# Kernel tuning notes

Hardware: AMD Instinct MI355X
Metric: run time of the kernel (lower is better)

## Reference

```python
import jax, jax.numpy as jnp
import numpy as np

BN_EPS = 1e-5


def _conv2d(x, w, b, pad):
    # x: [B,C,H,W], w: [O,I,kh,kw] (OIHW)
    y = jax.lax.conv_general_dilated(
        x, w, window_strides=(1, 1), padding=[(pad, pad), (pad, pad)],
        dimension_numbers=('NCHW', 'OIHW', 'NCHW'))
    return y + b[None, :, None, None]


def setup_inputs() -> dict:
    key = jax.random.key(0)
    ks = jax.random.split(key, 4)
    B, C, D, H, W = 8, 256, 1, 64, 64
    dm = 256
    x = jax.random.normal(ks[0], (B, C, D, H, W), dtype=jnp.float32)
    wq = jax.random.normal(ks[1], (dm, dm, 1, 1), dtype=jnp.float32) * 0.05
    bq = jnp.zeros((dm,), jnp.float32)
    wkv = jax.random.normal(ks[2], (2 * dm, dm, 3, 3), dtype=jnp.float32) * 0.05
    bkv = jnp.zeros((2 * dm,), jnp.float32)
    gamma = jnp.ones((dm,), jnp.float32)
    beta = jnp.zeros((dm,), jnp.float32)
    return {"x": x, "wq": wq, "bq": bq, "wkv": wkv, "bkv": bkv,
            "gamma": gamma, "beta": beta}


def reference(x, wq, bq, wkv, bkv, gamma, beta):
    B = x.shape[0]
    H, W = x.shape[-2], x.shape[-1]
    xc = x.reshape(B, -1, H, W)            # 'b c d h w -> b (c d) h w'
    dm = xc.shape[1]
    q = jax.nn.relu(_conv2d(xc, wq, bq, 0))       # [B,dm,H,W]
    kv = jax.nn.relu(_conv2d(xc, wkv, bkv, 1))    # [B,2dm,H,W]
    k, v = jnp.split(kv, 2, axis=1)

    def tok(t):  # 'b c x y -> b (x y) c'
        return t.transpose(0, 2, 3, 1).reshape(B, H * W, dm)

    qt, kt, vt = tok(q), tok(k), tok(v)
    sim = jnp.einsum('bid,bjd->bij', qt, kt)       # [B,N,N]
    A = jax.nn.softmax(sim / jnp.sqrt(jnp.float32(dm)), axis=-1)
    r = jnp.einsum('bij,bjd->bid', A, vt)          # [B,N,dm]
    r = r.reshape(B, H, W, dm).transpose(0, 3, 1, 2)  # 'b (x y) c -> b c x y'
    y = r + xc
    # BatchNorm2d, training mode: batch stats over (B,H,W), biased variance
    mean = jnp.mean(y, axis=(0, 2, 3), keepdims=True)
    var = jnp.var(y, axis=(0, 2, 3), keepdims=True)
    out = (y - mean) * jax.lax.rsqrt(var + BN_EPS)
    out = out * gamma[None, :, None, None] + beta[None, :, None, None]
    return out
```

## Files before the change

### kernel.cpp

```cpp
#include <hip/hip_runtime.h>


typedef __attribute__((ext_vector_type(8))) short bf16x8;
typedef __attribute__((ext_vector_type(4))) float f32x4;
typedef __attribute__((ext_vector_type(16))) float f32x16;
typedef __attribute__((ext_vector_type(8))) unsigned short u16x8;

__device__ inline unsigned short f2bf(float f) {
  union { float f; unsigned u; } c; c.f = f;
  unsigned u = c.u;
  return (unsigned short)((u + 0x7fffu + ((u >> 16) & 1u)) >> 16);
}

__device__ inline unsigned cvtpk(float lo, float hi) {
  unsigned r;
  asm("v_cvt_pk_bf16_f32 %0, %1, %2" : "=v"(r) : "v"(lo), "v"(hi));
  return r;
}

__device__ inline void dma16(const void* g, void* l) {
  __builtin_amdgcn_global_load_lds(
      (const __attribute__((address_space(1))) unsigned int*)g,
      (__attribute__((address_space(3))) unsigned int*)l, 16, 0, 0);
}

__global__ __launch_bounds__(256) void k_xt(
    const float* __restrict__ x, ushort* __restrict__ xt)
{
  const int b = blockIdx.z, ci0 = blockIdx.y * 64, gx = blockIdx.x;
  const int t = threadIdx.x;
  ushort* img = xt + (size_t)b * 4224 * 256;
  if (gx >= 64) {
    int r0 = (gx == 64) ? 0 : 4160;
#pragma unroll
    for (int k = 0; k < 2; ++k) {
      int idx = t + k * 256;
      int r = idx >> 3, u = idx & 7;
      u16x8 z = (u16x8)0;
      *(u16x8*)&img[(size_t)(r0 + r) * 256 + ci0 + u * 8] = z;
    }
    return;
  }
  const int n0 = gx * 64;
  __shared__ ushort tl[64][65];
  {
    const float* xb = x + ((size_t)b * 256 + ci0) * 4096 + n0;
    int i = t >> 2, j0 = (t & 3) * 16;
#pragma unroll
    for (int jj = 0; jj < 16; jj += 4) {
      float4 v = *(const float4*)&xb[(size_t)i * 4096 + j0 + jj];
      tl[j0 + jj + 0][i] = f2bf(v.x);
      tl[j0 + jj + 1][i] = f2bf(v.y);
      tl[j0 + jj + 2][i] = f2bf(v.z);
      tl[j0 + jj + 3][i] = f2bf(v.w);
    }
  }
  __syncthreads();
  {
    int j = t >> 3, u = t & 7;
#pragma unroll
    for (int k = 0; k < 2; ++k) {
      int jr = j + k * 32;
      ushort tmp[8];
#pragma unroll
      for (int e = 0; e < 8; ++e) tmp[e] = tl[jr][u * 8 + e];
      *(u16x8*)&img[(size_t)(64 + n0 + jr) * 256 + ci0 + u * 8] = *(u16x8*)tmp;
    }
  }
}

__global__ __launch_bounds__(256) void k_wprep(
    const float* __restrict__ w, ushort* __restrict__ wt, int ntaps, int nco)
{
  const int co = blockIdx.x;
  const int t = threadIdx.x;
  __shared__ float ws[2304];
  const int tot = 256 * ntaps;
  for (int i = t; i < tot; i += 256) ws[i] = w[(size_t)co * tot + i];
  __syncthreads();
  for (int tap = 0; tap < ntaps; ++tap)
    wt[((size_t)tap * nco + co) * 256 + t] = f2bf(ws[t * ntaps + tap]);
}

__global__ __launch_bounds__(256, 2) void k_conv(
    const ushort* __restrict__ xt, const ushort* __restrict__ wt,
    const float* __restrict__ bias, ushort* __restrict__ outT,
    ushort* __restrict__ outV, int ntaps, int nco, float oscale)
{
  extern __shared__ unsigned char smem[];
  ushort* As0 = (ushort*)smem;
  ushort* As1 = (ushort*)(smem + 16512);
  ushort* Bs0 = (ushort*)(smem + 33024);
  ushort* Bs1 = (ushort*)(smem + 33024 + 16384);
  __shared__ float bias_s[256];

  const int t = threadIdx.x, lane = t & 63;
  const int wv = t >> 6, wm = wv >> 1, wn = wv & 1;
  const int qc = lane & 15, grp = lane >> 4;
  const int b = blockIdx.z, n0 = blockIdx.x * 128, co0 = blockIdx.y * 256;
  const bool nchw = (outV != nullptr) && (blockIdx.y == 1);
  const ushort* img = xt + (size_t)b * 4224 * 256 + (size_t)64 * 256;
  const int wbase = t & ~63;

  bias_s[t] = bias[co0 + t];

  f32x4 acc[4][8];
#pragma unroll
  for (int mi = 0; mi < 4; ++mi)
#pragma unroll
    for (int ni = 0; ni < 8; ++ni) acc[mi][ni] = f32x4{0.f, 0.f, 0.f, 0.f};

  auto stageA = [&](int c8, ushort* dst) {
    const int ci0 = c8 * 32;
#pragma unroll
    for (int k = 0; k < 5; ++k) {
      int idx = k * 256 + t;
      if (idx < 1032) {
        int r = idx >> 2, u = idx & 3;
        int n = min(max(n0 + r - 65, -64), 4159);
        dma16(img + (size_t)n * 256 + ci0 + u * 8,
              dst + (size_t)(k * 256 + wbase) * 8);
      }
    }
  };
  auto stageB = [&](int tap, int c8, ushort* dst) {
    const ushort* wrow = wt + ((size_t)tap * nco + co0) * 256 + c8 * 32;
#pragma unroll
    for (int k = 0; k < 4; ++k) {
      int idx = k * 256 + t;
      int r = idx >> 2, u = idx & 3;
      dma16(wrow + (size_t)r * 256 + u * 8,
            dst + (size_t)(k * 256 + wbase) * 8);
    }
  };

  stageA(0, As0);
  stageB(0, 0, Bs0);
  asm volatile("s_waitcnt vmcnt(0)" ::: "memory");
  __syncthreads();

  const int niters = 8 * ntaps;
  int iter = 0;
  for (int c8 = 0; c8 < 8; ++c8) {
    const ushort* Asb = (c8 & 1) ? As1 : As0;
    for (int tap = 0; tap < ntaps; ++tap, ++iter) {
      const ushort* Bsb = (iter & 1) ? Bs1 : Bs0;
      if (iter + 1 < niters) {
        int ntap = (tap + 1 == ntaps) ? 0 : tap + 1;
        int nc8  = (tap + 1 == ntaps) ? c8 + 1 : c8;
        stageB(ntap, nc8, (iter & 1) ? Bs0 : Bs1);
        if (ntap == 0) stageA(nc8, (c8 & 1) ? As0 : As1);
      }
      const int dy = (ntaps == 9) ? (tap / 3 - 1) : 0;
      const int dx = (ntaps == 9) ? (tap % 3 - 1) : 0;
      const int off = dy * 64 + dx;
      bf16x8 bf[8];
#pragma unroll
      for (int ni = 0; ni < 8; ++ni)
        bf[ni] = *(const bf16x8*)&Bsb[(wn * 128 + ni * 16 + qc) * 32 + grp * 8];
#pragma unroll
      for (int mi = 0; mi < 4; ++mi) {
        int ar = wm * 64 + mi * 16 + qc + off + 65;
        bf16x8 af = *(const bf16x8*)&Asb[ar * 32 + grp * 8];
        if (dx < 0 && mi == 0 && qc == 0)  af = (bf16x8)0;
        if (dx > 0 && mi == 3 && qc == 15) af = (bf16x8)0;
#pragma unroll
        for (int ni = 0; ni < 8; ++ni)
          acc[mi][ni] = __builtin_amdgcn_mfma_f32_16x16x32_bf16(af, bf[ni], acc[mi][ni], 0, 0, 0);
      }
      asm volatile("s_waitcnt vmcnt(0)" ::: "memory");
      __syncthreads();
    }
  }

  if (!nchw) {
    ushort (*olds)[264] = (ushort(*)[264])smem;
#pragma unroll
    for (int mi = 0; mi < 4; ++mi) {
      int p = wm * 64 + mi * 16 + grp * 4;
#pragma unroll
      for (int ni = 0; ni < 8; ++ni) {
        int c = wn * 128 + ni * 16 + qc;
        float bv = bias_s[c];
#pragma unroll
        for (int r = 0; r < 4; ++r)
          olds[p + r][c] = f2bf(fmaxf(acc[mi][ni][r] + bv, 0.f) * oscale);
      }
    }
    __syncthreads();
    ushort* dst = outT + ((size_t)b * 4096 + n0) * 256;
#pragma unroll
    for (int k = 0; k < 16; ++k) {
      int idx = t + k * 256;
      int r = idx >> 5, u = idx & 31;
      *(u16x8*)&dst[(size_t)r * 256 + u * 8] = *(const u16x8*)&olds[r][u * 8];
    }
  } else {
    ushort (*oldsT)[136] = (ushort(*)[136])smem;
#pragma unroll
    for (int mi = 0; mi < 4; ++mi) {
      int p = wm * 64 + mi * 16 + grp * 4;
#pragma unroll
      for (int ni = 0; ni < 8; ++ni) {
        int c = wn * 128 + ni * 16 + qc;
        float bv = bias_s[c];
        ushort4 pk;
        pk.x = f2bf(fmaxf(acc[mi][ni][0] + bv, 0.f) * oscale);
        pk.y = f2bf(fmaxf(acc[mi][ni][1] + bv, 0.f) * oscale);
        pk.z = f2bf(fmaxf(acc[mi][ni][2] + bv, 0.f) * oscale);
        pk.w = f2bf(fmaxf(acc[mi][ni][3] + bv, 0.f) * oscale);
        *(ushort4*)&oldsT[c][p] = pk;
      }
    }
    __syncthreads();
    ushort* dst = outV + (size_t)b * 256 * 4096 + n0;
#pragma unroll
    for (int k = 0; k < 16; ++k) {
      int idx = t + k * 256;
      int c = idx >> 4, u = idx & 15;
      *(u16x8*)&dst[(size_t)c * 4096 + u * 8] = *(const u16x8*)&oldsT[c][u * 8];
    }
  }
}

__global__ __launch_bounds__(256, 1) void k_attn(
    const ushort* __restrict__ q_t, const ushort* __restrict__ k_t,
    const ushort* __restrict__ v_t, const float* __restrict__ x,
    float* __restrict__ y, float* __restrict__ gstat)
{
  extern __shared__ unsigned char smem[];
  ushort* kbf0 = (ushort*)smem;
  ushort* kbf1 = (ushort*)(smem + 32768);
  ushort* vbf0 = (ushort*)(smem + 65536);
  ushort* vbf1 = (ushort*)(smem + 98304);

  const int tid = threadIdx.x, lane = tid & 63, w = tid >> 6;
  const int q32 = lane & 31, gK = lane >> 5, swz = lane & 7;
  const int b = blockIdx.y, q0 = blockIdx.x * 128;
  const int wbase = tid & ~63;

  int offk[8], offv[8];
#pragma unroll
  for (int k = 0; k < 8; ++k) {
    int i = k * 256 + tid;
    int j = i >> 5, s = i & 31;
    offk[k] = j * 256 + ((s ^ (j & 7)) << 3);
    int d = i >> 3, s2 = i & 7;
    offv[k] = d * 4096 + ((s2 ^ (d & 7)) << 3);
  }
  const ushort* kT = k_t + (size_t)b * 4096 * 256;
  const ushort* vT = v_t + (size_t)b * 256 * 4096;

  bf16x8 qf[16];
  {
    const ushort* qrow =
        q_t + ((size_t)b * 4096 + q0 + w * 32 + q32) * 256 + gK * 8;
#pragma unroll
    for (int ds = 0; ds < 16; ++ds)
      qf[ds] = *(const bf16x8*)&qrow[ds * 16];
  }

  f32x16 o[8];
#pragma unroll
  for (int db = 0; db < 8; ++db) o[db] = (f32x16)0.f;
  float m_run = -1e30f, lp = 0.f;

  auto stage = [&](const ushort* kp, const ushort* vp, ushort* kb, ushort* vb) {
#pragma unroll
    for (int k = 0; k < 8; ++k)
      dma16(kp + offk[k], kb + (size_t)(k * 256 + wbase) * 8);
#pragma unroll
    for (int k = 0; k < 8; ++k)
      dma16(vp + offv[k], vb + (size_t)(k * 256 + wbase) * 8);
  };

  stage(kT, vT, kbf0, vbf0);
  kT += 16384; vT += 64;
  asm volatile("s_waitcnt vmcnt(0)" ::: "memory");
  __syncthreads();

  int kcol[16], vcol[4];
#pragma unroll
  for (int ds = 0; ds < 16; ++ds) kcol[ds] = ((2 * ds + gK) ^ swz) << 3;
#pragma unroll
  for (int ks = 0; ks < 4; ++ks) vcol[ks] = ((2 * ks + gK) ^ swz) << 3;
  const int krow0 = q32 * 256, krow1 = (q32 + 32) * 256;

  for (int t = 0; t < 64; ++t) {
    ushort* kb = (t & 1) ? kbf1 : kbf0;
    ushort* vb = (t & 1) ? vbf1 : vbf0;
    if (t < 63) {
      stage(kT, vT, (t & 1) ? kbf0 : kbf1, (t & 1) ? vbf0 : vbf1);
      kT += 16384; vT += 64;
    }

    f32x16 s0 = (f32x16)0.f, s1 = (f32x16)0.f;
    __builtin_amdgcn_s_setprio(1);
#pragma unroll
    for (int ds = 0; ds < 16; ++ds) {
      bf16x8 a0 = *(const bf16x8*)&kb[krow0 + kcol[ds]];
      bf16x8 a1 = *(const bf16x8*)&kb[krow1 + kcol[ds]];
      s0 = __builtin_amdgcn_mfma_f32_32x32x16_bf16(a0, qf[ds], s0, 0, 0, 0);
      s1 = __builtin_amdgcn_mfma_f32_32x32x16_bf16(a1, qf[ds], s1, 0, 0, 0);
    }
    __builtin_amdgcn_s_setprio(0);

    float pmax;
    {
      float m0 = fmaxf(fmaxf(s0[0], s0[1]), fmaxf(s0[2], s0[3]));
      m0 = fmaxf(m0, fmaxf(fmaxf(s0[4], s0[5]), fmaxf(s0[6], s0[7])));
      m0 = fmaxf(m0, fmaxf(fmaxf(s0[8], s0[9]), fmaxf(s0[10], s0[11])));
      m0 = fmaxf(m0, fmaxf(fmaxf(s0[12], s0[13]), fmaxf(s0[14], s0[15])));
      float m1 = fmaxf(fmaxf(s1[0], s1[1]), fmaxf(s1[2], s1[3]));
      m1 = fmaxf(m1, fmaxf(fmaxf(s1[4], s1[5]), fmaxf(s1[6], s1[7])));
      m1 = fmaxf(m1, fmaxf(fmaxf(s1[8], s1[9]), fmaxf(s1[10], s1[11])));
      m1 = fmaxf(m1, fmaxf(fmaxf(s1[12], s1[13]), fmaxf(s1[14], s1[15])));
      pmax = fmaxf(m0, m1);
    }
    pmax = fmaxf(pmax, __shfl_xor(pmax, 32));
    if (pmax - m_run > 11.5f) {
      float mn = fmaxf(m_run, pmax);
      float al = exp2f(m_run - mn);
      m_run = mn; lp *= al;
#pragma unroll
      for (int db = 0; db < 8; ++db) o[db] *= al;
    }
    float p0[16], p1[16];
#pragma unroll
    for (int r = 0; r < 16; ++r) {
      p0[r] = exp2f(s0[r] - m_run);
      p1[r] = exp2f(s1[r] - m_run);
      lp += p0[r] + p1[r];
    }

    bf16x8 pB[4];
    {
      unsigned a0 = cvtpk(p0[0], p0[1]),  a1 = cvtpk(p0[2], p0[3]);
      unsigned a2 = cvtpk(p0[4], p0[5]),  a3 = cvtpk(p0[6], p0[7]);
      unsigned a4 = cvtpk(p0[8], p0[9]),  a5 = cvtpk(p0[10], p0[11]);
      unsigned a6 = cvtpk(p0[12], p0[13]), a7 = cvtpk(p0[14], p0[15]);
      asm volatile("v_permlane32_swap_b32 %0, %1" : "+v"(a0), "+v"(a2));
      asm volatile("v_permlane32_swap_b32 %0, %1" : "+v"(a1), "+v"(a3));
      asm volatile("v_permlane32_swap_b32 %0, %1" : "+v"(a4), "+v"(a6));
      asm volatile("v_permlane32_swap_b32 %0, %1" : "+v"(a5), "+v"(a7));
      union { unsigned u[4]; bf16x8 v; } f0, f1;
      f0.u[0] = a0; f0.u[1] = a1; f0.u[2] = a2; f0.u[3] = a3;
      f1.u[0] = a4; f1.u[1] = a5; f1.u[2] = a6; f1.u[3] = a7;
      pB[0] = f0.v; pB[1] = f1.v;
      unsigned b0 = cvtpk(p1[0], p1[1]),  b1 = cvtpk(p1[2], p1[3]);
      unsigned b2 = cvtpk(p1[4], p1[5]),  b3 = cvtpk(p1[6], p1[7]);
      unsigned b4 = cvtpk(p1[8], p1[9]),  b5 = cvtpk(p1[10], p1[11]);
      unsigned b6 = cvtpk(p1[12], p1[13]), b7 = cvtpk(p1[14], p1[15]);
      asm volatile("v_permlane32_swap_b32 %0, %1" : "+v"(b0), "+v"(b2));
      asm volatile("v_permlane32_swap_b32 %0, %1" : "+v"(b1), "+v"(b3));
      asm volatile("v_permlane32_swap_b32 %0, %1" : "+v"(b4), "+v"(b6));
      asm volatile("v_permlane32_swap_b32 %0, %1" : "+v"(b5), "+v"(b7));
      union { unsigned u[4]; bf16x8 v; } f2, f3;
      f2.u[0] = b0; f2.u[1] = b1; f2.u[2] = b2; f2.u[3] = b3;
      f3.u[0] = b4; f3.u[1] = b5; f3.u[2] = b6; f3.u[3] = b7;
      pB[2] = f2.v; pB[3] = f3.v;
    }

    __builtin_amdgcn_s_setprio(1);
#pragma unroll
    for (int db = 0; db < 8; ++db) {
      const int vbase = (db * 32 + q32) * 64;
#pragma unroll
      for (int ks = 0; ks < 4; ++ks) {
        bf16x8 va = *(const bf16x8*)&vb[vbase + vcol[ks]];
        o[db] = __builtin_amdgcn_mfma_f32_32x32x16_bf16(va, pB[ks], o[db], 0, 0, 0);
      }
    }
    __builtin_amdgcn_s_setprio(0);

    asm volatile("s_waitcnt vmcnt(0)" ::: "memory");
    __syncthreads();
  }

  lp += __shfl_xor(lp, 32);
  float inv = 1.f / lp;

  float (*obuf)[132] = (float(*)[132])smem;
  float* part1 = (float*)(smem + 135168);
  float* part2 = (float*)(smem + 136192);
#pragma unroll
  for (int db = 0; db < 8; ++db)
#pragma unroll
    for (int r = 0; r < 16; ++r) {
      int d = db * 32 + (r & 3) + 8 * (r >> 2) + 4 * gK;
      obuf[d][w * 32 + q32] = o[db][r] * inv;
    }
  __syncthreads();

  const float* xb = x + (size_t)b * 256 * 4096 + q0;
  float*       yb = y + (size_t)b * 256 * 4096 + q0;
#pragma unroll
  for (int k = 0; k < 32; ++k) {
    int i = tid + k * 256;
    int c = i >> 5, f4 = (i & 31) << 2;
    float4 xr4 = *(const float4*)&xb[(size_t)c * 4096 + f4];
    float4 rv = *(const float4*)&obuf[c][f4];
    rv.x += xr4.x; rv.y += xr4.y; rv.z += xr4.z; rv.w += xr4.w;
    *(float4*)&yb[(size_t)c * 4096 + f4] = rv;
    float ls1 = (rv.x + rv.y) + (rv.z + rv.w);
    float ls2 = (rv.x * rv.x + rv.y * rv.y) + (rv.z * rv.z + rv.w * rv.w);
#pragma unroll
    for (int sh = 1; sh <= 16; sh <<= 1) {
      ls1 += __shfl_xor(ls1, sh);
      ls2 += __shfl_xor(ls2, sh);
    }
    if ((tid & 31) == 0) { part1[c] = ls1; part2[c] = ls2; }
  }
  __syncthreads();
  atomicAdd(&gstat[tid], part1[tid]);
  atomicAdd(&gstat[256 + tid], part2[tid]);
}

__global__ __launch_bounds__(256) void k_bnapply(
    float* __restrict__ y, const float* __restrict__ gstat,
    const float* __restrict__ gamma, const float* __restrict__ beta)
{
  __shared__ float sc_s[256], sh_s[256];
  {
    const int c = threadIdx.x;
    float mean = gstat[c] * (1.f / 32768.f);
    float var  = gstat[256 + c] * (1.f / 32768.f) - mean * mean;
    float inv  = rsqrtf(var + 1e-5f);
    float g = gamma[c] * inv;
    sc_s[c] = g;
    sh_s[c] = beta[c] - mean * g;
  }
  __syncthreads();
  const int total4 = 8 * 256 * 1024;
  for (int i = blockIdx.x * 256 + threadIdx.x; i < total4; i += gridDim.x * 256) {
    int c = (i >> 10) & 255;
    float sc = sc_s[c], sh = sh_s[c];
    float4 v = ((const float4*)y)[i];
    v.x = fmaf(v.x, sc, sh);
    v.y = fmaf(v.y, sc, sh);
    v.z = fmaf(v.z, sc, sh);
    v.w = fmaf(v.w, sc, sh);
    ((float4*)y)[i] = v;
  }
}

extern "C" void kernel_launch(void* const* d_in, const int* in_sizes, int n_in,
                              void* d_out, int out_size, void* d_ws, size_t ws_size,
                              hipStream_t stream) {
  const float* x     = (const float*)d_in[0];
  const float* wq    = (const float*)d_in[1];
  const float* bq    = (const float*)d_in[2];
  const float* wkv   = (const float*)d_in[3];
  const float* bkv   = (const float*)d_in[4];
  const float* gamma = (const float*)d_in[5];
  const float* beta  = (const float*)d_in[6];
  float* out = (float*)d_out;

  ushort* xt  = (ushort*)d_ws;
  ushort* wt3 = xt  + (size_t)8650752;
  ushort* wt1 = wt3 + (size_t)1179648;
  ushort* q_t = wt1 + (size_t)65536;
  ushort* k_t = q_t + (size_t)8388608;
  ushort* v_t = k_t + (size_t)8388608;
  float* gstat = (float*)(v_t + (size_t)8388608);

  hipMemsetAsync(gstat, 0, 2048, stream);

  k_xt<<<dim3(66, 4, 8), 256, 0, stream>>>(x, xt);
  k_wprep<<<dim3(512), 256, 0, stream>>>(wkv, wt3, 9, 512);
  k_wprep<<<dim3(256), 256, 0, stream>>>(wq, wt1, 1, 256);

  const int conv_smem = 69632;
  hipFuncSetAttribute(reinterpret_cast<const void*>(k_conv),
                      hipFuncAttributeMaxDynamicSharedMemorySize, conv_smem);
  k_conv<<<dim3(32, 1, 8), 256, conv_smem, stream>>>(
      xt, wt1, bq, q_t, nullptr, 1, 256, 0.0625f * 1.44269504f);
  k_conv<<<dim3(32, 2, 8), 256, conv_smem, stream>>>(
      xt, wt3, bkv, k_t, v_t, 9, 512, 1.0f);

  const int attn_smem = 147456;
  hipFuncSetAttribute(reinterpret_cast<const void*>(k_attn),
                      hipFuncAttributeMaxDynamicSharedMemorySize, attn_smem);
  k_attn<<<dim3(32, 8), 256, attn_smem, stream>>>(q_t, k_t, v_t, x, out, gstat);

  k_bnapply<<<dim3(2048), 256, 0, stream>>>(out, gstat, gamma, beta);
}
```

Measured before the change: 328.6 us.

## Split attention key range across two wave groups per block and merge softmax states

Doubles the attention block to 512 threads, with two groups of four waves each streaming half of the keys using smaller 32-key tiles. At the end, the running max, sum and output accumulators of the two groups are combined through shared memory before the residual add and batch-stat reduction. The aim is more resident waves per CU to hide load and softmax latency. In exchange it adds a cross-group merge, halves the MFMA work per wave per iteration, and tightens the register budget under the new launch bounds.

New measurement: 624.5 us. 1.9x slower.

```diff
diff --git a/kernel.cpp b/kernel.cpp
--- a/kernel.cpp
+++ b/kernel.cpp
@@ -223,38 +223,38 @@
   }
 }
 
-__global__ __launch_bounds__(256, 1) void k_attn(
+__global__ __launch_bounds__(512, 2) void k_attn(
     const ushort* __restrict__ q_t, const ushort* __restrict__ k_t,
     const ushort* __restrict__ v_t, const float* __restrict__ x,
     float* __restrict__ y, float* __restrict__ gstat)
 {
   extern __shared__ unsigned char smem[];
-  ushort* kbf0 = (ushort*)smem;
-  ushort* kbf1 = (ushort*)(smem + 32768);
-  ushort* vbf0 = (ushort*)(smem + 65536);
-  ushort* vbf1 = (ushort*)(smem + 98304);
-
   const int tid = threadIdx.x, lane = tid & 63, w = tid >> 6;
-  const int q32 = lane & 31, gK = lane >> 5, swz = lane & 7;
+  const int g = w >> 2, wg = w & 3, tg = tid & 255;
+  const int q32 = lane & 31, gK = lane >> 5, swz = q32 & 7;
   const int b = blockIdx.y, q0 = blockIdx.x * 128;
-  const int wbase = tid & ~63;
-
-  int offk[8], offv[8];
-#pragma unroll
-  for (int k = 0; k < 8; ++k) {
-    int i = k * 256 + tid;
+
+  ushort* kbf[2] = { (ushort*)(smem + g * 32768),
+                     (ushort*)(smem + g * 32768 + 16384) };
+  ushort* vbf[2] = { (ushort*)(smem + 65536 + g * 32768),
+                     (ushort*)(smem + 65536 + g * 32768 + 16384) };
+
+  int offk[4], offv[4];
+#pragma unroll
+  for (int k = 0; k < 4; ++k) {
+    int i = k * 256 + tg;
     int j = i >> 5, s = i & 31;
     offk[k] = j * 256 + ((s ^ (j & 7)) << 3);
-    int d = i >> 3, s2 = i & 7;
-    offv[k] = d * 4096 + ((s2 ^ (d & 7)) << 3);
-  }
-  const ushort* kT = k_t + (size_t)b * 4096 * 256;
-  const ushort* vT = v_t + (size_t)b * 256 * 4096;
+    int d = i >> 2, s2 = i & 3;
+    offv[k] = d * 4096 + ((s2 ^ (d & 3)) << 3);
+  }
+  const ushort* kT = k_t + ((size_t)b * 4096 + g * 2048) * 256;
+  const ushort* vT = v_t + (size_t)b * 256 * 4096 + g * 2048;
 
   bf16x8 qf[16];
   {
     const ushort* qrow =
-        q_t + ((size_t)b * 4096 + q0 + w * 32 + q32) * 256 + gK * 8;
+        q_t + ((size_t)b * 4096 + q0 + wg * 32 + q32) * 256 + gK * 8;
 #pragma unroll
     for (int ds = 0; ds < 16; ++ds)
       qf[ds] = *(const bf16x8*)&qrow[ds * 16];
@@ -267,41 +267,39 @@
 
   auto stage = [&](const ushort* kp, const ushort* vp, ushort* kb, ushort* vb) {
 #pragma unroll
-    for (int k = 0; k < 8; ++k)
-      dma16(kp + offk[k], kb + (size_t)(k * 256 + wbase) * 8);
-#pragma unroll
-    for (int k = 0; k < 8; ++k)
-      dma16(vp + offv[k], vb + (size_t)(k * 256 + wbase) * 8);
+    for (int k = 0; k < 4; ++k)
+      dma16(kp + offk[k], kb + (size_t)(k * 256 + wg * 64) * 8);
+#pragma unroll
+    for (int k = 0; k < 4; ++k)
+      dma16(vp + offv[k], vb + (size_t)(k * 256 + wg * 64) * 8);
   };
 
-  stage(kT, vT, kbf0, vbf0);
-  kT += 16384; vT += 64;
+  stage(kT, vT, kbf[0], vbf[0]);
+  kT += 8192; vT += 32;
   asm volatile("s_waitcnt vmcnt(0)" ::: "memory");
   __syncthreads();
 
-  int kcol[16], vcol[4];
+  int kcol[16], vcol[2];
 #pragma unroll
   for (int ds = 0; ds < 16; ++ds) kcol[ds] = ((2 * ds + gK) ^ swz) << 3;
 #pragma unroll
-  for (int ks = 0; ks < 4; ++ks) vcol[ks] = ((2 * ks + gK) ^ swz) << 3;
-  const int krow0 = q32 * 256, krow1 = (q32 + 32) * 256;
+  for (int ks = 0; ks < 2; ++ks) vcol[ks] = ((2 * ks + gK) ^ (q32 & 3)) << 3;
+  const int krow = q32 * 256;
 
   for (int t = 0; t < 64; ++t) {
-    ushort* kb = (t & 1) ? kbf1 : kbf0;
-    ushort* vb = (t & 1) ? vbf1 : vbf0;
+    ushort* kb = kbf[t & 1];
+    ushort* vb = vbf[t & 1];
     if (t < 63) {
-      stage(kT, vT, (t & 1) ? kbf0 : kbf1, (t & 1) ? vbf0 : vbf1);
-      kT += 16384; vT += 64;
-    }
-
-    f32x16 s0 = (f32x16)0.f, s1 = (f32x16)0.f;
+      stage(kT, vT, kbf[(t + 1) & 1], vbf[(t + 1) & 1]);
+      kT += 8192; vT += 32;
+    }
+
+    f32x16 s0 = (f32x16)0.f;
     __builtin_amdgcn_s_setprio(1);
 #pragma unroll
     for (int ds = 0; ds < 16; ++ds) {
-      bf16x8 a0 = *(const bf16x8*)&kb[krow0 + kcol[ds]];
-      bf16x8 a1 = *(const bf16x8*)&kb[krow1 + kcol[ds]];
+      bf16x8 a0 = *(const bf16x8*)&kb[krow + kcol[ds]];
       s0 = __builtin_amdgcn_mfma_f32_32x32x16_bf16(a0, qf[ds], s0, 0, 0, 0);
-      s1 = __builtin_amdgcn_mfma_f32_32x32x16_bf16(a1, qf[ds], s1, 0, 0, 0);
     }
     __builtin_amdgcn_s_setprio(0);
 
@@ -311,11 +309,7 @@
       m0 = fmaxf(m0, fmaxf(fmaxf(s0[4], s0[5]), fmaxf(s0[6], s0[7])));
       m0 = fmaxf(m0, fmaxf(fmaxf(s0[8], s0[9]), fmaxf(s0[10], s0[11])));
       m0 = fmaxf(m0, fmaxf(fmaxf(s0[12], s0[13]), fmaxf(s0[14], s0[15])));
-      float m1 = fmaxf(fmaxf(s1[0], s1[1]), fmaxf(s1[2], s1[3]));
-      m1 = fmaxf(m1, fmaxf(fmaxf(s1[4], s1[5]), fmaxf(s1[6], s1[7])));
-      m1 = fmaxf(m1, fmaxf(fmaxf(s1[8], s1[9]), fmaxf(s1[10], s1[11])));
-      m1 = fmaxf(m1, fmaxf(fmaxf(s1[12], s1[13]), fmaxf(s1[14], s1[15])));
-      pmax = fmaxf(m0, m1);
+      pmax = m0;
     }
     pmax = fmaxf(pmax, __shfl_xor(pmax, 32));
     if (pmax - m_run > 11.5f) {
@@ -325,15 +319,14 @@
 #pragma unroll
       for (int db = 0; db < 8; ++db) o[db] *= al;
     }
-    float p0[16], p1[16];
+    float p0[16];
 #pragma unroll
     for (int r = 0; r < 16; ++r) {
       p0[r] = exp2f(s0[r] - m_run);
-      p1[r] = exp2f(s1[r] - m_run);
-      lp += p0[r] + p1[r];
-    }
-
-    bf16x8 pB[4];
+      lp += p0[r];
+    }
+
+    bf16x8 pB[2];
     {
       unsigned a0 = cvtpk(p0[0], p0[1]),  a1 = cvtpk(p0[2], p0[3]);
       unsigned a2 = cvtpk(p0[4], p0[5]),  a3 = cvtpk(p0[6], p0[7]);
@@ -347,29 +340,16 @@
       f0.u[0] = a0; f0.u[1] = a1; f0.u[2] = a2; f0.u[3] = a3;
       f1.u[0] = a4; f1.u[1] = a5; f1.u[2] = a6; f1.u[3] = a7;
       pB[0] = f0.v; pB[1] = f1.v;
-      unsigned b0 = cvtpk(p1[0], p1[1]),  b1 = cvtpk(p1[2], p1[3]);
-      unsigned b2 = cvtpk(p1[4], p1[5]),  b3 = cvtpk(p1[6], p1[7]);
-      unsigned b4 = cvtpk(p1[8], p1[9]),  b5 = cvtpk(p1[10], p1[11]);
-      unsigned b6 = cvtpk(p1[12], p1[13]), b7 = cvtpk(p1[14], p1[15]);
-      asm volatile("v_permlane32_swap_b32 %0, %1" : "+v"(b0), "+v"(b2));
-      asm volatile("v_permlane32_swap_b32 %0, %1" : "+v"(b1), "+v"(b3));
-      asm volatile("v_permlane32_swap_b32 %0, %1" : "+v"(b4), "+v"(b6));
-      asm volatile("v_permlane32_swap_b32 %0, %1" : "+v"(b5), "+v"(b7));
-      union { unsigned u[4]; bf16x8 v; } f2, f3;
-      f2.u[0] = b0; f2.u[1] = b1; f2.u[2] = b2; f2.u[3] = b3;
-      f3.u[0] = b4; f3.u[1] = b5; f3.u[2] = b6; f3.u[3] = b7;
-      pB[2] = f2.v; pB[3] = f3.v;
     }
 
     __builtin_amdgcn_s_setprio(1);
 #pragma unroll
     for (int db = 0; db < 8; ++db) {
-      const int vbase = (db * 32 + q32) * 64;
-#pragma unroll
-      for (int ks = 0; ks < 4; ++ks) {
-        bf16x8 va = *(const bf16x8*)&vb[vbase + vcol[ks]];
-        o[db] = __builtin_amdgcn_mfma_f32_32x32x16_bf16(va, pB[ks], o[db], 0, 0, 0);
-      }
+      const int vbase = (db * 32 + q32) * 32;
+      bf16x8 va0 = *(const bf16x8*)&vb[vbase + vcol[0]];
+      bf16x8 va1 = *(const bf16x8*)&vb[vbase + vcol[1]];
+      o[db] = __builtin_amdgcn_mfma_f32_32x32x16_bf16(va0, pB[0], o[db], 0, 0, 0);
+      o[db] = __builtin_amdgcn_mfma_f32_32x32x16_bf16(va1, pB[1], o[db], 0, 0, 0);
     }
     __builtin_amdgcn_s_setprio(0);
 
@@ -378,25 +358,46 @@
   }
 
   lp += __shfl_xor(lp, 32);
-  float inv = 1.f / lp;
+
+  float2* mlbuf = (float2*)(smem + 135168);
+  float* part1  = (float*)(smem + 137216);
+  float* part2  = (float*)(smem + 138240);
+  if (gK == 0) mlbuf[w * 32 + q32] = make_float2(m_run, lp);
+  __syncthreads();
+  float2 mp = mlbuf[(w ^ 4) * 32 + q32];
+  float mF = fmaxf(m_run, mp.x);
+  float aS = exp2f(m_run - mF);
+  float lf = lp * aS + mp.y * exp2f(mp.x - mF);
+  float inv = 1.f / lf;
 
   float (*obuf)[132] = (float(*)[132])smem;
-  float* part1 = (float*)(smem + 135168);
-  float* part2 = (float*)(smem + 136192);
-#pragma unroll
-  for (int db = 0; db < 8; ++db)
-#pragma unroll
-    for (int r = 0; r < 16; ++r) {
-      int d = db * 32 + (r & 3) + 8 * (r >> 2) + 4 * gK;
-      obuf[d][w * 32 + q32] = o[db][r] * inv;
-    }
+  if (g == 1) {
+#pragma unroll
+    for (int db = 0; db < 8; ++db)
+#pragma unroll
+      for (int r = 0; r < 16; ++r) {
+        int d = db * 32 + (r & 3) + 8 * (r >> 2) + 4 * gK;
+        obuf[d][wg * 32 + q32] = o[db][r] * aS;
+      }
+  }
+  __syncthreads();
+  if (g == 0) {
+#pragma unroll
+    for (int db = 0; db < 8; ++db)
+#pragma unroll
+      for (int r = 0; r < 16; ++r) {
+        int d = db * 32 + (r & 3) + 8 * (r >> 2) + 4 * gK;
+        obuf[d][wg * 32 + q32] =
+            (o[db][r] * aS + obuf[d][wg * 32 + q32]) * inv;
+      }
+  }
   __syncthreads();
 
   const float* xb = x + (size_t)b * 256 * 4096 + q0;
   float*       yb = y + (size_t)b * 256 * 4096 + q0;
 #pragma unroll
-  for (int k = 0; k < 32; ++k) {
-    int i = tid + k * 256;
+  for (int k = 0; k < 16; ++k) {
+    int i = tid + k * 512;
     int c = i >> 5, f4 = (i & 31) << 2;
     float4 xr4 = *(const float4*)&xb[(size_t)c * 4096 + f4];
     float4 rv = *(const float4*)&obuf[c][f4];
@@ -412,8 +413,10 @@
     if ((tid & 31) == 0) { part1[c] = ls1; part2[c] = ls2; }
   }
   __syncthreads();
-  atomicAdd(&gstat[tid], part1[tid]);
-  atomicAdd(&gstat[256 + tid], part2[tid]);
+  if (tid < 256) {
+    atomicAdd(&gstat[tid], part1[tid]);
+    atomicAdd(&gstat[256 + tid], part2[tid]);
+  }
 }
 
 __global__ __launch_bounds__(256) void k_bnapply(
@@ -478,10 +481,10 @@
   k_conv<<<dim3(32, 2, 8), 256, conv_smem, stream>>>(
       xt, wt3, bkv, k_t, v_t, 9, 512, 1.0f);
 
-  const int attn_smem = 147456;
+  const int attn_smem = 139264;
   hipFuncSetAttribute(reinterpret_cast<const void*>(k_attn),
                       hipFuncAttributeMaxDynamicSharedMemorySize, attn_smem);
-  k_attn<<<dim3(32, 8), 256, attn_smem, stream>>>(q_t, k_t, v_t, x, out, gstat);
+  k_attn<<<dim3(32, 8), 512, attn_smem, stream>>>(q_t, k_t, v_t, x, out, gstat);
 
   k_bnapply<<<dim3(2048), 256, 0, stream>>>(out, gstat, gamma, beta);
 }
```
